# Kernel optimization log

Measured on AMD Instinct MI355X. Metric: run time of the kernel, lower is better.

The kernel has to match this reference:

```python
import jax, jax.numpy as jnp
import numpy as np

B, S, D, H, K, R = 16, 512, 768, 12, 16, 32
NS = 128  # LSH sample size = min(128, S//2)
HD = D // H

def _ln(t, g, b):
    m = t.mean(-1, keepdims=True)
    v = t.var(-1, keepdims=True)
    return (t - m) / jnp.sqrt(v + 1e-5) * g + b

def setup_inputs() -> dict:
    key = jax.random.key(0)
    ks = jax.random.split(key, 16)
    n = lambda k, shp: jax.random.normal(k, shp, jnp.float32) * 0.02
    return {
        'x': jax.random.normal(ks[0], (B, S, D), jnp.float32),
        'sample_idx': jax.random.randint(ks[1], (NS,), 0, S, jnp.int32),
        'w1': n(ks[2], (6, D // 4)), 'b1': jnp.zeros(D // 4, jnp.float32),
        'w2': n(ks[3], (D // 4, R)), 'b2': jnp.zeros(R, jnp.float32),
        'wd0': n(ks[4], (R, R)), 'bd0': jnp.zeros(R, jnp.float32),
        'wd1': n(ks[5], (R, R)), 'bd1': jnp.zeros(R, jnp.float32),
        'in_proj_w': n(ks[6], (D, 3 * D)), 'in_proj_b': jnp.zeros(3 * D, jnp.float32),
        'out_proj_w': n(ks[7], (D, D)), 'out_proj_b': jnp.zeros(D, jnp.float32),
        'topo_w': n(ks[8], (R, D)), 'topo_b': jnp.zeros(D, jnp.float32),
        'topo_gate': jnp.float32(0.1),
        'ln1_g': jnp.ones(D, jnp.float32), 'ln1_b': jnp.zeros(D, jnp.float32),
        'ln2_g': jnp.ones(D, jnp.float32), 'ln2_b': jnp.zeros(D, jnp.float32),
        'ffn_w1': n(ks[9], (D, 2 * D)), 'ffn_b1': jnp.zeros(2 * D, jnp.float32),
        'ffn_w2': n(ks[10], (2 * D, D)), 'ffn_b2': jnp.zeros(D, jnp.float32),
    }

def reference(x, sample_idx, w1, b1, w2, b2, wd0, bd0, wd1, bd1,
              in_proj_w, in_proj_b, out_proj_w, out_proj_b,
              topo_w, topo_b, topo_gate, ln1_g, ln1_b, ln2_g, ln2_b,
              ffn_w1, ffn_b1, ffn_w2, ffn_b2):
    # --- FastLSH._lsh_knn (S > 256 path): cdist to 128 sampled tokens + topk smallest ---
    s = jnp.take(x, sample_idx, axis=1)                                   # [B,NS,D]
    d2 = (jnp.sum(x * x, -1)[:, :, None] + jnp.sum(s * s, -1)[:, None, :]
          - 2.0 * jnp.einsum('bnd,bmd->bnm', x, s))                       # [B,S,NS]
    dist = jnp.sqrt(jnp.maximum(d2, 0.0))
    neg_top, _nbr = jax.lax.top_k(-dist, K)
    knn_dist = -neg_top                                                   # [B,S,K]
    # --- SimplifiedPersistenceComputer: scalar stats per batch (torch uses .item(), detached) ---
    df = knn_dist.reshape(B, -1)
    mean = df.mean(1); std = df.std(1, ddof=1)                            # torch.std is unbiased
    mn = df.min(1); mx = df.max(1)
    stats0 = jax.lax.stop_gradient(
        jnp.stack([mean, std, mn, mx, mean / 2, std / 2], -1))            # [B,6]
    # --- FastPersistenceLandscape: only dim-0 landscape feeds attention ---
    land0 = (jax.nn.relu(stats0 @ w1 + b1) @ w2 + b2) @ wd0 + bd0         # [B,R]
    # --- TopologicalAttention: MHA self-attention + gated topo embedding ---
    qkv = x @ in_proj_w + in_proj_b                                       # [B,S,3D]
    q, k, v = jnp.split(qkv, 3, axis=-1)
    hsplit = lambda t: t.reshape(B, S, H, HD).transpose(0, 2, 1, 3)
    q, k, v = hsplit(q), hsplit(k), hsplit(v)
    p = jax.nn.softmax(jnp.einsum('bhqd,bhkd->bhqk', q, k) / jnp.sqrt(jnp.float32(HD)), -1)
    o = jnp.einsum('bhqk,bhkd->bhqd', p, v).transpose(0, 2, 1, 3).reshape(B, S, D)
    attn = o @ out_proj_w + out_proj_b
    topo = land0 @ topo_w + topo_b                                        # [B,D]
    attn_out = attn + topo_gate * topo[:, None, :]
    # --- post-norm residual + FFN (GELU exact) ---
    x1 = _ln(x + attn_out, ln1_g, ln1_b)
    ffn = jax.nn.gelu(x1 @ ffn_w1 + ffn_b1, approximate=False) @ ffn_w2 + ffn_b2
    return _ln(x1 + ffn, ln2_g, ln2_b)
```

## Files before the change

### kernel.cpp

```cpp
#include <hip/hip_runtime.h>
#include <math.h>

#define Bz 16
#define Sz 512
#define Dz 768
#define Hz 12
#define HDz 64
#define Kz 16
#define NSz 128
#define Rz 32

typedef __attribute__((ext_vector_type(4))) float f32x4;
typedef __attribute__((ext_vector_type(8))) short bf16x8;

__device__ __forceinline__ unsigned short f2bf(float f) {
    unsigned u = __float_as_uint(f);
    return (unsigned short)((u + 0x7fffu + ((u >> 16) & 1u)) >> 16);
}
__device__ __forceinline__ float bf2f(unsigned short s) {
    return __uint_as_float(((unsigned)s) << 16);
}
__device__ __forceinline__ unsigned pk2(float a, float b) {
    return (unsigned)f2bf(a) | ((unsigned)f2bf(b) << 16);
}
__device__ __forceinline__ void gload_lds16(const void* g, void* l) {
    __builtin_amdgcn_global_load_lds(
        (const __attribute__((address_space(1))) unsigned int*)g,
        (__attribute__((address_space(3))) unsigned int*)l, 16, 0, 0);
}

__global__ __launch_bounds__(256) void xrn_k(const float* __restrict__ x, short* __restrict__ xb,
                                             float* __restrict__ xsq) {
    int wv = threadIdx.x >> 6, lane = threadIdx.x & 63;
    int row = blockIdx.x * 4 + wv;
    const float* r = x + (size_t)row * Dz;
    unsigned long long* dst = (unsigned long long*)(xb + (size_t)row * Dz);
    float s = 0.f;
#pragma unroll
    for (int j = 0; j < 3; j++) {
        float4 v = ((const float4*)r)[lane + j * 64];
        s += v.x * v.x + v.y * v.y + v.z * v.z + v.w * v.w;
        dst[lane + j * 64] = (unsigned long long)pk2(v.x, v.y) | ((unsigned long long)pk2(v.z, v.w) << 32);
    }
#pragma unroll
    for (int off = 32; off > 0; off >>= 1) s += __shfl_xor(s, off, 64);
    if (lane == 0) xsq[row] = s;
}

__global__ __launch_bounds__(256) void wtrans_k(const float* __restrict__ src, short* __restrict__ dst,
                                                int K, int N) {
    __shared__ float t[64][65];
    int k0 = blockIdx.y * 64, n0 = blockIdx.x * 64;
#pragma unroll
    for (int i = 0; i < 16; i++) {
        int e = threadIdx.x + 256 * i;
        int kk = e >> 6, nn = e & 63;
        t[kk][nn] = src[(size_t)(k0 + kk) * N + n0 + nn];
    }
    __syncthreads();
#pragma unroll
    for (int i = 0; i < 16; i++) {
        int e = threadIdx.x + 256 * i;
        int nn = e >> 6, kk = e & 63;
        dst[(size_t)(n0 + nn) * K + k0 + kk] = (short)f2bf(t[kk][nn]);
    }
}

__global__ __launch_bounds__(256) void dist_k(const float* __restrict__ x, const int* __restrict__ sidx,
                                              const float* __restrict__ xsq, float* __restrict__ D) {
    __shared__ float Xs[16][65];
    __shared__ float Ss[16][65];
    int b = blockIdx.z, st = blockIdx.y, jt = blockIdx.x;
    int tx = threadIdx.x & 15, ty = threadIdx.x >> 4;
    const float* xb = x + (size_t)b * Sz * Dz;
    float acc[4][4] = {};
    for (int k0 = 0; k0 < Dz; k0 += 16) {
#pragma unroll
        for (int i = 0; i < 4; i++) {
            int e = threadIdx.x + 256 * i;
            int m = e >> 4, kk = e & 15;
            Xs[kk][m] = xb[(size_t)(st * 64 + m) * Dz + k0 + kk];
            Ss[kk][m] = xb[(size_t)sidx[jt * 64 + m] * Dz + k0 + kk];
        }
        __syncthreads();
#pragma unroll
        for (int kk = 0; kk < 16; kk++) {
            float a[4], bb[4];
#pragma unroll
            for (int i = 0; i < 4; i++) a[i] = Xs[kk][ty * 4 + i];
#pragma unroll
            for (int j = 0; j < 4; j++) bb[j] = Ss[kk][tx * 4 + j];
#pragma unroll
            for (int i = 0; i < 4; i++)
#pragma unroll
                for (int j = 0; j < 4; j++) acc[i][j] += a[i] * bb[j];
        }
        __syncthreads();
    }
#pragma unroll
    for (int i = 0; i < 4; i++) {
        int s = st * 64 + ty * 4 + i;
#pragma unroll
        for (int j = 0; j < 4; j++) {
            int jj = jt * 64 + tx * 4 + j;
            float d2 = xsq[b * Sz + s] + xsq[b * Sz + sidx[jj]] - 2.f * acc[i][j];
            D[((size_t)b * Sz + s) * NSz + jj] = sqrtf(fmaxf(d2, 0.f));
        }
    }
}

__global__ __launch_bounds__(128) void knnstat_k(const float* __restrict__ D, float4* __restrict__ rowred) {
    __shared__ float dv[NSz];
    __shared__ float red[NSz], red2[NSz];
    __shared__ float rmin, rmax;
    int tid = threadIdx.x, row = blockIdx.x;
    float dist = D[(size_t)row * NSz + tid];
    dv[tid] = dist;
    __syncthreads();
    int rank = 0;
#pragma unroll 8
    for (int j = 0; j < NSz; j++) {
        float o = dv[j];
        rank += (o < dist) || (o == dist && j < tid);
    }
    if (rank == 0) rmin = dist;
    if (rank == Kz - 1) rmax = dist;
    red[tid] = (rank < Kz) ? dist : 0.f;
    red2[tid] = (rank < Kz) ? dist * dist : 0.f;
    __syncthreads();
    for (int st = 64; st > 0; st >>= 1) {
        if (tid < st) { red[tid] += red[tid + st]; red2[tid] += red2[tid + st]; }
        __syncthreads();
    }
    if (tid == 0) rowred[row] = make_float4(red[0], red2[0], rmin, rmax);
}

__global__ __launch_bounds__(256) void land_topo_k(const float4* __restrict__ rowred,
                                                   const float* __restrict__ w1, const float* __restrict__ b1,
                                                   const float* __restrict__ w2, const float* __restrict__ b2,
                                                   const float* __restrict__ wd0, const float* __restrict__ bd0,
                                                   const float* __restrict__ topo_w, const float* __restrict__ topo_b,
                                                   const float* gate, float* __restrict__ topo_add) {
    __shared__ float4 red4[256];
    __shared__ float st[6];
    __shared__ float h[Dz / 4];
    __shared__ float l2[Rz];
    __shared__ float land[Rz];
    int b = blockIdx.x, tid = threadIdx.x;
    float4 a = rowred[b * Sz + tid];
    float4 c = rowred[b * Sz + 256 + tid];
    float4 r;
    r.x = a.x + c.x; r.y = a.y + c.y;
    r.z = fminf(a.z, c.z); r.w = fmaxf(a.w, c.w);
    red4[tid] = r;
    __syncthreads();
    for (int stp = 128; stp > 0; stp >>= 1) {
        if (tid < stp) {
            float4 p = red4[tid], q = red4[tid + stp];
            p.x += q.x; p.y += q.y; p.z = fminf(p.z, q.z); p.w = fmaxf(p.w, q.w);
            red4[tid] = p;
        }
        __syncthreads();
    }
    if (tid == 0) {
        const double N = (double)(Sz * Kz);
        double sum = (double)red4[0].x, sumsq = (double)red4[0].y;
        double mean = sum / N;
        double var = (sumsq - N * mean * mean) / (N - 1.0);
        float sd = (float)sqrt(fmax(var, 0.0));
        float m = (float)mean;
        st[0] = m; st[1] = sd;
        st[2] = red4[0].z; st[3] = red4[0].w;
        st[4] = m * 0.5f; st[5] = sd * 0.5f;
    }
    __syncthreads();
    if (tid < Dz / 4) {
        float a1 = b1[tid];
#pragma unroll
        for (int i = 0; i < 6; i++) a1 += st[i] * w1[i * (Dz / 4) + tid];
        h[tid] = fmaxf(a1, 0.f);
    }
    __syncthreads();
    if (tid < Rz) {
        float a1 = b2[tid];
        for (int i = 0; i < Dz / 4; i++) a1 += h[i] * w2[i * Rz + tid];
        l2[tid] = a1;
    }
    __syncthreads();
    if (tid < Rz) {
        float a1 = bd0[tid];
#pragma unroll
        for (int i = 0; i < Rz; i++) a1 += l2[i] * wd0[i * Rz + tid];
        land[tid] = a1;
    }
    __syncthreads();
    float g = gate[0];
    for (int d = tid; d < Dz; d += 256) {
        float a1 = topo_b[d];
#pragma unroll
        for (int i = 0; i < Rz; i++) a1 += land[i] * topo_w[i * Dz + d];
        topo_add[b * Dz + d] = g * a1;
    }
}

__device__ __forceinline__ void stage_tile(const short* gbase, int ldk, int row0, int k0,
                                           short* ldsbase, int w, int l) {
#pragma unroll
    for (int c = 0; c < 2; c++) {
        int r = c * 64 + w * 16 + (l >> 2);
        int qg = (l & 3) ^ ((r >> 1) & 3);
        const short* src = gbase + (size_t)(row0 + r) * ldk + k0 + qg * 8;
        gload_lds16(src, ldsbase + (c * 4 + w) * 512);
    }
}

template <int EPI>
__global__ __launch_bounds__(256) void mgemm_k(const short* __restrict__ A, const short* __restrict__ BT,
                                               const float* __restrict__ bias,
                                               float* __restrict__ C, short* __restrict__ Cb,
                                               int N, int Kd,
                                               short* __restrict__ qo, short* __restrict__ ko,
                                               short* __restrict__ vT) {
    __shared__ short lds[2][2][4096];
    int tid = threadIdx.x, w = tid >> 6, l = tid & 63;
    int m0 = blockIdx.y * 128, n0 = blockIdx.x * 128;
    int wr = w >> 1, wc = w & 1, g = l >> 4, ql = l & 15;
    f32x4 acc[4][4];
#pragma unroll
    for (int i = 0; i < 4; i++)
#pragma unroll
        for (int j = 0; j < 4; j++) acc[i][j] = (f32x4){0.f, 0.f, 0.f, 0.f};
    stage_tile(A, Kd, m0, 0, lds[0][0], w, l);
    stage_tile(BT, Kd, n0, 0, lds[0][1], w, l);
    __syncthreads();
    int nst = Kd / 32;
    for (int t = 0; t < nst; t++) {
        int buf = t & 1;
        if (t + 1 < nst) {
            stage_tile(A, Kd, m0, (t + 1) * 32, lds[buf ^ 1][0], w, l);
            stage_tile(BT, Kd, n0, (t + 1) * 32, lds[buf ^ 1][1], w, l);
        }
        bf16x8 af[4], bfr[4];
#pragma unroll
        for (int i = 0; i < 4; i++) {
            int r = wr * 64 + i * 16 + ql;
            af[i] = *(const bf16x8*)((const char*)lds[buf][0] + r * 64 + ((g ^ ((r >> 1) & 3)) << 4));
        }
#pragma unroll
        for (int j = 0; j < 4; j++) {
            int r = wc * 64 + j * 16 + ql;
            bfr[j] = *(const bf16x8*)((const char*)lds[buf][1] + r * 64 + ((g ^ ((r >> 1) & 3)) << 4));
        }
#pragma unroll
        for (int i = 0; i < 4; i++)
#pragma unroll
            for (int j = 0; j < 4; j++)
                acc[i][j] = __builtin_amdgcn_mfma_f32_16x16x32_bf16(af[i], bfr[j], acc[i][j], 0, 0, 0);
        __syncthreads();
    }

    if (EPI == 0) {
#pragma unroll
        for (int i = 0; i < 4; i++) {
            int rowb = m0 + wr * 64 + i * 16 + g * 4;
#pragma unroll
            for (int j = 0; j < 4; j++) {
                int col = n0 + wc * 64 + j * 16 + ql;
                float bsv = bias[col];
#pragma unroll
                for (int r = 0; r < 4; r++)
                    C[(size_t)(rowb + r) * N + col] = acc[i][j][r] + bsv;
            }
        }
    } else {
        short* cl = (short*)lds;
        const int part = (EPI == 2) ? (n0 / Dz) : 0;
        const bool cm = (EPI == 2) && (part == 2);
        if (!cm) {
#pragma unroll
            for (int i = 0; i < 4; i++) {
#pragma unroll
                for (int j = 0; j < 4; j++) {
                    int colL = wc * 64 + j * 16 + ql;
                    float bsv = bias[n0 + colL];
#pragma unroll
                    for (int r = 0; r < 4; r++) {
                        int rowL = wr * 64 + i * 16 + g * 4 + r;
                        float val = acc[i][j][r] + bsv;
                        if (EPI == 1) val = 0.5f * val * (1.f + erff(val * 0.70710678118654752f));
                        cl[rowL * 128 + (((colL >> 3) ^ (rowL & 15)) << 3) + (colL & 7)] = (short)f2bf(val);
                    }
                }
            }
        } else {
#pragma unroll
            for (int i = 0; i < 4; i++) {
#pragma unroll
                for (int j = 0; j < 4; j++) {
                    int colL = wc * 64 + j * 16 + ql;
                    float bsv = bias[n0 + colL];
                    int row4 = wr * 64 + i * 16 + g * 4;
                    unsigned long long u =
                        (unsigned long long)pk2(acc[i][j][0] + bsv, acc[i][j][1] + bsv)
                      | ((unsigned long long)pk2(acc[i][j][2] + bsv, acc[i][j][3] + bsv) << 32);
                    *(unsigned long long*)((char*)cl +
                        colL * 256 + (((row4 >> 3) ^ (colL & 15)) << 4) + (row4 & 7) * 2) = u;
                }
            }
        }
        __syncthreads();
#pragma unroll
        for (int it = 0; it < 8; it++) {
            int c = tid + 256 * it;
            int a = c >> 4, sl = c & 15;
            bf16x8 vv = *(const bf16x8*)(cl + a * 128 + ((sl ^ (a & 15)) << 3));
            if (EPI == 1) {
                *(bf16x8*)(Cb + (size_t)(m0 + a) * N + n0 + sl * 8) = vv;
            } else if (!cm) {
                int rr = m0 + a;
                int b = rr >> 9, s = rr & 511;
                int h = ((n0 % Dz) >> 6) + (sl >> 3);
                short* dst = part ? ko : qo;
                *(bf16x8*)(dst + (((size_t)(b * Hz + h)) * Sz + s) * HDz + (sl & 7) * 8) = vv;
            } else {
                int wi = (n0 - 2 * Dz) + a;
                int h = wi >> 6, hd = wi & 63;
                int b = m0 >> 9, s0 = (m0 & 511) + sl * 8;
                *(bf16x8*)(vT + ((size_t)(b * Hz + h) * HDz + hd) * Sz + s0) = vv;
            }
        }
    }
}

__global__ __launch_bounds__(256, 4) void attn4_k(const short* __restrict__ Q, const short* __restrict__ Kt,
                                                  const short* __restrict__ Vt, short* __restrict__ O) {
    __shared__ short kl[2][4096];
    __shared__ short vl[2][4096];
    __shared__ char plds[4][2048];
    int tid = threadIdx.x, w = tid >> 6, l = tid & 63;
    int bh = blockIdx.x % (Bz * Hz), qt = blockIdx.x / (Bz * Hz);
    int g = l >> 4, ql = l & 15;
    const short* qb = Q + (size_t)bh * (Sz * HDz) + (size_t)(qt * 64 + w * 16) * HDz;
    const short* kb = Kt + (size_t)bh * (Sz * HDz);
    const short* vb = Vt + (size_t)bh * (HDz * Sz);
    bf16x8 qf0 = *(const bf16x8*)(qb + (size_t)ql * HDz + g * 8);
    bf16x8 qf1 = *(const bf16x8*)(qb + (size_t)ql * HDz + 32 + g * 8);
    f32x4 oa[4];
#pragma unroll
    for (int m = 0; m < 4; m++) oa[m] = (f32x4){0.f, 0.f, 0.f, 0.f};
    float psum = 0.f;

    auto stage = [&](int c, int bb) {
#pragma unroll
        for (int it = 0; it < 2; it++) {
            int i = (it * 4 + w) * 64 + l;
            int row = i >> 3;
            int ss = (i & 7) ^ (row & 7);
            gload_lds16(kb + (size_t)(c * 64 + row) * HDz + ss * 8,
                        (char*)kl[bb] + (it * 4 + w) * 1024);
            gload_lds16(vb + (size_t)row * Sz + c * 64 + ss * 8,
                        (char*)vl[bb] + (it * 4 + w) * 1024);
        }
    };

    stage(0, 0);
    __syncthreads();
    char* pw = plds[w];
#pragma unroll
    for (int c = 0; c < 8; c++) {
        int cur = c & 1;
        if (c < 7) stage(c + 1, cur ^ 1);
        const char* kc = (const char*)kl[cur];
        const char* vc = (const char*)vl[cur];
#pragma unroll
        for (int tl = 0; tl < 4; tl++) {
            int row = tl * 16 + ql;
            bf16x8 a0 = *(const bf16x8*)(kc + row * 128 + ((g ^ (ql & 7)) << 4));
            bf16x8 a1 = *(const bf16x8*)(kc + row * 128 + (((4 + g) ^ (ql & 7)) << 4));
            f32x4 s4 = (f32x4){0.f, 0.f, 0.f, 0.f};
            s4 = __builtin_amdgcn_mfma_f32_16x16x32_bf16(a0, qf0, s4, 0, 0, 0);
            s4 = __builtin_amdgcn_mfma_f32_16x16x32_bf16(a1, qf1, s4, 0, 0, 0);
            float e0 = __expf(s4[0] * 0.125f);
            float e1 = __expf(s4[1] * 0.125f);
            float e2 = __expf(s4[2] * 0.125f);
            float e3 = __expf(s4[3] * 0.125f);
            psum += (e0 + e1) + (e2 + e3);
            int slot = (tl * 2 + (g >> 1)) ^ (ql & 7);
            *(unsigned long long*)(pw + ql * 128 + slot * 16 + (g & 1) * 8)
                = (unsigned long long)pk2(e0, e1) | ((unsigned long long)pk2(e2, e3) << 32);
        }
#pragma unroll
        for (int s = 0; s < 2; s++) {
            int slot = (s * 4 + g) ^ (ql & 7);
            bf16x8 pb = *(const bf16x8*)(pw + ql * 128 + slot * 16);
#pragma unroll
            for (int m = 0; m < 4; m++) {
                int row = m * 16 + ql;
                bf16x8 va = *(const bf16x8*)(vc + row * 128 + (((s * 4 + g) ^ (ql & 7)) << 4));
                oa[m] = __builtin_amdgcn_mfma_f32_16x16x32_bf16(va, pb, oa[m], 0, 0, 0);
            }
        }
        __syncthreads();
    }
    psum += __shfl_xor(psum, 16, 64);
    psum += __shfl_xor(psum, 32, 64);
    float inv = 1.f / psum;
    int b = bh / Hz, h = bh % Hz;
    int s = qt * 64 + w * 16 + ql;
#pragma unroll
    for (int m = 0; m < 4; m++)
#pragma unroll
        for (int j = 0; j < 2; j++) {
            float v0 = oa[m][j * 2] * inv, v1 = oa[m][j * 2 + 1] * inv;
            unsigned u = pk2(v0, v1);
            int d = h * 64 + m * 16 + g * 4 + j * 2;
            *(unsigned*)((char*)O + 2 * ((size_t)(b * Sz + s) * Dz + d)) = u;
        }
}

__global__ __launch_bounds__(256) void ln1_k(const float* __restrict__ x, const float* __restrict__ ap,
                                             const float* __restrict__ topo,
                                             const float* __restrict__ gam, const float* __restrict__ bet,
                                             short* __restrict__ x1b) {
    __shared__ float buf[Dz];
    __shared__ float red[256];
    int row = blockIdx.x, tid = threadIdx.x, b = row >> 9;
    float s = 0.f;
    for (int i = tid; i < Dz; i += 256) {
        float vv = x[(size_t)row * Dz + i] + ap[(size_t)row * Dz + i] + topo[b * Dz + i];
        buf[i] = vv; s += vv;
    }
    red[tid] = s; __syncthreads();
    for (int st = 128; st > 0; st >>= 1) { if (tid < st) red[tid] += red[tid + st]; __syncthreads(); }
    float mean = red[0] / (float)Dz;
    __syncthreads();
    float s2 = 0.f;
    for (int i = tid; i < Dz; i += 256) { float d = buf[i] - mean; s2 += d * d; }
    red[tid] = s2; __syncthreads();
    for (int st = 128; st > 0; st >>= 1) { if (tid < st) red[tid] += red[tid + st]; __syncthreads(); }
    float inv = 1.f / sqrtf(red[0] / (float)Dz + 1e-5f);
    for (int i = tid; i < Dz; i += 256)
        x1b[(size_t)row * Dz + i] = (short)f2bf((buf[i] - mean) * inv * gam[i] + bet[i]);
}

__global__ __launch_bounds__(256) void ln2_k(const short* __restrict__ x1b, const float* __restrict__ f2,
                                             const float* __restrict__ gam, const float* __restrict__ bet,
                                             float* __restrict__ out) {
    __shared__ float buf[Dz];
    __shared__ float red[256];
    int row = blockIdx.x, tid = threadIdx.x;
    float s = 0.f;
    for (int i = tid; i < Dz; i += 256) {
        float vv = bf2f((unsigned short)x1b[(size_t)row * Dz + i]) + f2[(size_t)row * Dz + i];
        buf[i] = vv; s += vv;
    }
    red[tid] = s; __syncthreads();
    for (int st = 128; st > 0; st >>= 1) { if (tid < st) red[tid] += red[tid + st]; __syncthreads(); }
    float mean = red[0] / (float)Dz;
    __syncthreads();
    float s2 = 0.f;
    for (int i = tid; i < Dz; i += 256) { float d = buf[i] - mean; s2 += d * d; }
    red[tid] = s2; __syncthreads();
    for (int st = 128; st > 0; st >>= 1) { if (tid < st) red[tid] += red[tid + st]; __syncthreads(); }
    float inv = 1.f / sqrtf(red[0] / (float)Dz + 1e-5f);
    for (int i = tid; i < Dz; i += 256)
        out[(size_t)row * Dz + i] = (buf[i] - mean) * inv * gam[i] + bet[i];
}

extern "C" void kernel_launch(void* const* d_in, const int* in_sizes, int n_in,
                              void* d_out, int out_size, void* d_ws, size_t ws_size,
                              hipStream_t stream) {
    const float* x          = (const float*)d_in[0];
    const int*   sidx       = (const int*)d_in[1];
    const float* w1         = (const float*)d_in[2];
    const float* b1         = (const float*)d_in[3];
    const float* w2         = (const float*)d_in[4];
    const float* b2         = (const float*)d_in[5];
    const float* wd0        = (const float*)d_in[6];
    const float* bd0        = (const float*)d_in[7];
    const float* in_proj_w  = (const float*)d_in[10];
    const float* in_proj_b  = (const float*)d_in[11];
    const float* out_proj_w = (const float*)d_in[12];
    const float* out_proj_b = (const float*)d_in[13];
    const float* topo_w     = (const float*)d_in[14];
    const float* topo_b     = (const float*)d_in[15];
    const float* gate       = (const float*)d_in[16];
    const float* ln1_g      = (const float*)d_in[17];
    const float* ln1_b      = (const float*)d_in[18];
    const float* ln2_g      = (const float*)d_in[19];
    const float* ln2_b      = (const float*)d_in[20];
    const float* ffn_w1     = (const float*)d_in[21];
    const float* ffn_b1     = (const float*)d_in[22];
    const float* ffn_w2     = (const float*)d_in[23];
    const float* ffn_b2     = (const float*)d_in[24];

    char* w = (char*)d_ws;
    float4* rowred = (float4*)(w + 0);
    float*  xsq    = (float*)(w + 131072);
    float*  topo_add = (float*)(w + 163840);
    size_t off = 212992;
    short* wT_ip = (short*)(w + off); off += (size_t)3 * Dz * Dz * 2;
    short* wT_op = (short*)(w + off); off += (size_t)Dz * Dz * 2;
    short* wT_f1 = (short*)(w + off); off += (size_t)2 * Dz * Dz * 2;
    short* wT_f2 = (short*)(w + off); off += (size_t)2 * Dz * Dz * 2;
    float* Dd    = (float*)(w + off); off += (size_t)Bz * Sz * NSz * 4;
    char*  qkv0  = w + off;           off += (size_t)3 * Bz * Sz * Dz * 2;
    short* qbuf  = (short*)qkv0;
    short* kbuf  = (short*)(qkv0 + (size_t)Bz * Sz * Dz * 2);
    short* vTbuf = (short*)(qkv0 + (size_t)2 * Bz * Sz * Dz * 2);
    short* x1b   = (short*)qkv0;
    short* hb    = (short*)(qkv0 + (size_t)Bz * Sz * Dz * 2);
    short* xb    = (short*)(w + off); off += (size_t)Bz * Sz * Dz * 2;
    short* ob    = xb;
    float* bigF  = (float*)(w + off); off += (size_t)Bz * Sz * Dz * 4;

    const int M = Bz * Sz;

    xrn_k<<<M / 4, 256, 0, stream>>>(x, xb, xsq);
    wtrans_k<<<dim3(3 * Dz / 64, Dz / 64), 256, 0, stream>>>(in_proj_w, wT_ip, Dz, 3 * Dz);
    wtrans_k<<<dim3(Dz / 64, Dz / 64), 256, 0, stream>>>(out_proj_w, wT_op, Dz, Dz);
    wtrans_k<<<dim3(2 * Dz / 64, Dz / 64), 256, 0, stream>>>(ffn_w1, wT_f1, Dz, 2 * Dz);
    wtrans_k<<<dim3(Dz / 64, 2 * Dz / 64), 256, 0, stream>>>(ffn_w2, wT_f2, 2 * Dz, Dz);
    dist_k<<<dim3(NSz / 64, Sz / 64, Bz), 256, 0, stream>>>(x, sidx, xsq, Dd);
    knnstat_k<<<M, 128, 0, stream>>>(Dd, rowred);
    land_topo_k<<<Bz, 256, 0, stream>>>(rowred, w1, b1, w2, b2,
                                        wd0, bd0, topo_w, topo_b, gate, topo_add);
    mgemm_k<2><<<dim3(3 * Dz / 128, M / 128), 256, 0, stream>>>(xb, wT_ip, in_proj_b,
                                                                nullptr, nullptr, 3 * Dz, Dz,
                                                                qbuf, kbuf, vTbuf);
    attn4_k<<<Bz * Hz * 8, 256, 0, stream>>>(qbuf, kbuf, vTbuf, ob);
    mgemm_k<0><<<dim3(Dz / 128, M / 128), 256, 0, stream>>>(ob, wT_op, out_proj_b,
                                                            bigF, nullptr, Dz, Dz,
                                                            nullptr, nullptr, nullptr);
    ln1_k<<<M, 256, 0, stream>>>(x, bigF, topo_add, ln1_g, ln1_b, x1b);
    mgemm_k<1><<<dim3(2 * Dz / 128, M / 128), 256, 0, stream>>>(x1b, wT_f1, ffn_b1,
                                                                nullptr, hb, 2 * Dz, Dz,
                                                                nullptr, nullptr, nullptr);
    mgemm_k<0><<<dim3(Dz / 128, M / 128), 256, 0, stream>>>(hb, wT_f2, ffn_b2,
                                                            bigF, nullptr, Dz, 2 * Dz,
                                                            nullptr, nullptr, nullptr);
    ln2_k<<<M, 256, 0, stream>>>(x1b, bigF, ln2_g, ln2_b, (float*)d_out);
}
```

Before: 444.4 us.

## Merge prep kernels, use MFMA GEMM for distances, XCD-swizzle tiles, bf16 GEMM outputs

Merges the four weight-transpose launches and a gather of the sampled tokens into bf16 into a single prep kernel. The fp32 CUDA-core cdist kernel is replaced by the bf16 MFMA GEMM, with a new epilogue that computes sqrt distances. GEMM launches become 1D grids with a block-index remap that spreads consecutive tiles across the eight XCDs, and the out-proj and FFN2 outputs are stored as bf16 instead of fp32 to halve that traffic. The bf16 distance products may reorder near-tied neighbours in top-k, and the bf16 residual inputs slightly reduce accuracy.

```diff
diff --git a/kernel.cpp b/kernel.cpp
--- a/kernel.cpp
+++ b/kernel.cpp
@@ -47,64 +47,56 @@
     if (lane == 0) xsq[row] = s;
 }
 
-__global__ __launch_bounds__(256) void wtrans_k(const float* __restrict__ src, short* __restrict__ dst,
-                                                int K, int N) {
-    __shared__ float t[64][65];
-    int k0 = blockIdx.y * 64, n0 = blockIdx.x * 64;
+__device__ __forceinline__ void wtrans_body(const float* __restrict__ src, short* __restrict__ dst,
+                                            int K, int N, int k0, int n0, int tid,
+                                            float (*t)[65]) {
 #pragma unroll
     for (int i = 0; i < 16; i++) {
-        int e = threadIdx.x + 256 * i;
+        int e = tid + 256 * i;
         int kk = e >> 6, nn = e & 63;
         t[kk][nn] = src[(size_t)(k0 + kk) * N + n0 + nn];
     }
     __syncthreads();
 #pragma unroll
     for (int i = 0; i < 16; i++) {
-        int e = threadIdx.x + 256 * i;
+        int e = tid + 256 * i;
         int nn = e >> 6, kk = e & 63;
         dst[(size_t)(n0 + nn) * K + k0 + kk] = (short)f2bf(t[kk][nn]);
     }
 }
 
-__global__ __launch_bounds__(256) void dist_k(const float* __restrict__ x, const int* __restrict__ sidx,
-                                              const float* __restrict__ xsq, float* __restrict__ D) {
-    __shared__ float Xs[16][65];
-    __shared__ float Ss[16][65];
-    int b = blockIdx.z, st = blockIdx.y, jt = blockIdx.x;
-    int tx = threadIdx.x & 15, ty = threadIdx.x >> 4;
-    const float* xb = x + (size_t)b * Sz * Dz;
-    float acc[4][4] = {};
-    for (int k0 = 0; k0 < Dz; k0 += 16) {
-#pragma unroll
-        for (int i = 0; i < 4; i++) {
-            int e = threadIdx.x + 256 * i;
-            int m = e >> 4, kk = e & 15;
-            Xs[kk][m] = xb[(size_t)(st * 64 + m) * Dz + k0 + kk];
-            Ss[kk][m] = xb[(size_t)sidx[jt * 64 + m] * Dz + k0 + kk];
-        }
-        __syncthreads();
-#pragma unroll
-        for (int kk = 0; kk < 16; kk++) {
-            float a[4], bb[4];
-#pragma unroll
-            for (int i = 0; i < 4; i++) a[i] = Xs[kk][ty * 4 + i];
-#pragma unroll
-            for (int j = 0; j < 4; j++) bb[j] = Ss[kk][tx * 4 + j];
-#pragma unroll
-            for (int i = 0; i < 4; i++)
-#pragma unroll
-                for (int j = 0; j < 4; j++) acc[i][j] += a[i] * bb[j];
-        }
-        __syncthreads();
-    }
-#pragma unroll
-    for (int i = 0; i < 4; i++) {
-        int s = st * 64 + ty * 4 + i;
-#pragma unroll
-        for (int j = 0; j < 4; j++) {
-            int jj = jt * 64 + tx * 4 + j;
-            float d2 = xsq[b * Sz + s] + xsq[b * Sz + sidx[jj]] - 2.f * acc[i][j];
-            D[((size_t)b * Sz + s) * NSz + jj] = sqrtf(fmaxf(d2, 0.f));
+__global__ __launch_bounds__(256) void prep_k(const float* __restrict__ ipw, const float* __restrict__ opw,
+                                              const float* __restrict__ f1w, const float* __restrict__ f2w,
+                                              short* __restrict__ wT_ip, short* __restrict__ wT_op,
+                                              short* __restrict__ wT_f1, short* __restrict__ wT_f2,
+                                              const float* __restrict__ x, const int* __restrict__ sidx,
+                                              short* __restrict__ scb) {
+    __shared__ float t[64][65];
+    int bid = blockIdx.x, tid = threadIdx.x;
+    if (bid < 432) {
+        int lo = bid, tx = lo % 36, ty = lo / 36;
+        wtrans_body(ipw, wT_ip, Dz, 3 * Dz, ty * 64, tx * 64, tid, t);
+    } else if (bid < 576) {
+        int lo = bid - 432, tx = lo % 12, ty = lo / 12;
+        wtrans_body(opw, wT_op, Dz, Dz, ty * 64, tx * 64, tid, t);
+    } else if (bid < 864) {
+        int lo = bid - 576, tx = lo % 24, ty = lo / 24;
+        wtrans_body(f1w, wT_f1, Dz, 2 * Dz, ty * 64, tx * 64, tid, t);
+    } else if (bid < 1152) {
+        int lo = bid - 864, tx = lo % 12, ty = lo / 12;
+        wtrans_body(f2w, wT_f2, 2 * Dz, Dz, ty * 64, tx * 64, tid, t);
+    } else {
+        int gb = bid - 1152;
+        int row = gb * 16 + (tid >> 4);
+        int b = row >> 7, jj = row & 127;
+        const float* src = x + ((size_t)(b * Sz) + sidx[jj]) * Dz;
+        unsigned long long* dr = (unsigned long long*)(scb + (size_t)row * Dz);
+        int l16 = tid & 15;
+#pragma unroll
+        for (int j = 0; j < 12; j++) {
+            int idx = j * 16 + l16;
+            float4 v = ((const float4*)src)[idx];
+            dr[idx] = (unsigned long long)pk2(v.x, v.y) | ((unsigned long long)pk2(v.z, v.w) << 32);
         }
     }
 }
@@ -218,12 +210,17 @@
 __global__ __launch_bounds__(256) void mgemm_k(const short* __restrict__ A, const short* __restrict__ BT,
                                                const float* __restrict__ bias,
                                                float* __restrict__ C, short* __restrict__ Cb,
-                                               int N, int Kd,
+                                               int N, int Kd, int gx,
                                                short* __restrict__ qo, short* __restrict__ ko,
-                                               short* __restrict__ vT) {
+                                               short* __restrict__ vT,
+                                               const int* __restrict__ sidx, const float* __restrict__ xsq) {
     __shared__ short lds[2][2][4096];
     int tid = threadIdx.x, w = tid >> 6, l = tid & 63;
-    int m0 = blockIdx.y * 128, n0 = blockIdx.x * 128;
+    int nwg = gridDim.x, q = nwg >> 3;
+    int orig = (blockIdx.x & 7) * q + (blockIdx.x >> 3);
+    int m0 = (orig / gx) * 128, n0 = (orig % gx) * 128;
+    const short* BTb = BT;
+    if (EPI == 4) BTb += (size_t)(m0 >> 9) * NSz * Kd;
     int wr = w >> 1, wc = w & 1, g = l >> 4, ql = l & 15;
     f32x4 acc[4][4];
 #pragma unroll
@@ -231,14 +228,14 @@
 #pragma unroll
         for (int j = 0; j < 4; j++) acc[i][j] = (f32x4){0.f, 0.f, 0.f, 0.f};
     stage_tile(A, Kd, m0, 0, lds[0][0], w, l);
-    stage_tile(BT, Kd, n0, 0, lds[0][1], w, l);
+    stage_tile(BTb, Kd, n0, 0, lds[0][1], w, l);
     __syncthreads();
     int nst = Kd / 32;
     for (int t = 0; t < nst; t++) {
         int buf = t & 1;
         if (t + 1 < nst) {
             stage_tile(A, Kd, m0, (t + 1) * 32, lds[buf ^ 1][0], w, l);
-            stage_tile(BT, Kd, n0, (t + 1) * 32, lds[buf ^ 1][1], w, l);
+            stage_tile(BTb, Kd, n0, (t + 1) * 32, lds[buf ^ 1][1], w, l);
         }
         bf16x8 af[4], bfr[4];
 #pragma unroll
@@ -259,17 +256,20 @@
         __syncthreads();
     }
 
-    if (EPI == 0) {
+    if (EPI == 4) {
 #pragma unroll
         for (int i = 0; i < 4; i++) {
             int rowb = m0 + wr * 64 + i * 16 + g * 4;
 #pragma unroll
             for (int j = 0; j < 4; j++) {
-                int col = n0 + wc * 64 + j * 16 + ql;
-                float bsv = bias[col];
-#pragma unroll
-                for (int r = 0; r < 4; r++)
-                    C[(size_t)(rowb + r) * N + col] = acc[i][j][r] + bsv;
+                int col = wc * 64 + j * 16 + ql;
+                float ssq = xsq[((rowb >> 9) << 9) + sidx[col]];
+#pragma unroll
+                for (int r = 0; r < 4; r++) {
+                    int row = rowb + r;
+                    float d2 = xsq[row] + ssq - 2.f * acc[i][j][r];
+                    C[(size_t)row * NSz + col] = sqrtf(fmaxf(d2, 0.f));
+                }
             }
         }
     } else {
@@ -314,7 +314,7 @@
             int c = tid + 256 * it;
             int a = c >> 4, sl = c & 15;
             bf16x8 vv = *(const bf16x8*)(cl + a * 128 + ((sl ^ (a & 15)) << 3));
-            if (EPI == 1) {
+            if (EPI == 1 || EPI == 3) {
                 *(bf16x8*)(Cb + (size_t)(m0 + a) * N + n0 + sl * 8) = vv;
             } else if (!cm) {
                 int rr = m0 + a;
@@ -418,7 +418,7 @@
         }
 }
 
-__global__ __launch_bounds__(256) void ln1_k(const float* __restrict__ x, const float* __restrict__ ap,
+__global__ __launch_bounds__(256) void ln1_k(const float* __restrict__ x, const short* __restrict__ ap,
                                              const float* __restrict__ topo,
                                              const float* __restrict__ gam, const float* __restrict__ bet,
                                              short* __restrict__ x1b) {
@@ -427,7 +427,7 @@
     int row = blockIdx.x, tid = threadIdx.x, b = row >> 9;
     float s = 0.f;
     for (int i = tid; i < Dz; i += 256) {
-        float vv = x[(size_t)row * Dz + i] + ap[(size_t)row * Dz + i] + topo[b * Dz + i];
+        float vv = x[(size_t)row * Dz + i] + bf2f((unsigned short)ap[(size_t)row * Dz + i]) + topo[b * Dz + i];
         buf[i] = vv; s += vv;
     }
     red[tid] = s; __syncthreads();
@@ -443,7 +443,7 @@
         x1b[(size_t)row * Dz + i] = (short)f2bf((buf[i] - mean) * inv * gam[i] + bet[i]);
 }
 
-__global__ __launch_bounds__(256) void ln2_k(const short* __restrict__ x1b, const float* __restrict__ f2,
+__global__ __launch_bounds__(256) void ln2_k(const short* __restrict__ x1b, const short* __restrict__ f2,
                                              const float* __restrict__ gam, const float* __restrict__ bet,
                                              float* __restrict__ out) {
     __shared__ float buf[Dz];
@@ -451,7 +451,7 @@
     int row = blockIdx.x, tid = threadIdx.x;
     float s = 0.f;
     for (int i = tid; i < Dz; i += 256) {
-        float vv = bf2f((unsigned short)x1b[(size_t)row * Dz + i]) + f2[(size_t)row * Dz + i];
+        float vv = bf2f((unsigned short)x1b[(size_t)row * Dz + i]) + bf2f((unsigned short)f2[(size_t)row * Dz + i]);
         buf[i] = vv; s += vv;
     }
     red[tid] = s; __syncthreads();
@@ -503,6 +503,7 @@
     short* wT_op = (short*)(w + off); off += (size_t)Dz * Dz * 2;
     short* wT_f1 = (short*)(w + off); off += (size_t)2 * Dz * Dz * 2;
     short* wT_f2 = (short*)(w + off); off += (size_t)2 * Dz * Dz * 2;
+    short* scb   = (short*)(w + off); off += (size_t)Bz * NSz * Dz * 2;
     float* Dd    = (float*)(w + off); off += (size_t)Bz * Sz * NSz * 4;
     char*  qkv0  = w + off;           off += (size_t)3 * Bz * Sz * Dz * 2;
     short* qbuf  = (short*)qkv0;
@@ -512,32 +513,32 @@
     short* hb    = (short*)(qkv0 + (size_t)Bz * Sz * Dz * 2);
     short* xb    = (short*)(w + off); off += (size_t)Bz * Sz * Dz * 2;
     short* ob    = xb;
-    float* bigF  = (float*)(w + off); off += (size_t)Bz * Sz * Dz * 4;
+    short* apb   = (short*)(w + off); off += (size_t)Bz * Sz * Dz * 2;
+    short* f2b   = (short*)(w + off); off += (size_t)Bz * Sz * Dz * 2;
 
     const int M = Bz * Sz;
 
     xrn_k<<<M / 4, 256, 0, stream>>>(x, xb, xsq);
-    wtrans_k<<<dim3(3 * Dz / 64, Dz / 64), 256, 0, stream>>>(in_proj_w, wT_ip, Dz, 3 * Dz);
-    wtrans_k<<<dim3(Dz / 64, Dz / 64), 256, 0, stream>>>(out_proj_w, wT_op, Dz, Dz);
-    wtrans_k<<<dim3(2 * Dz / 64, Dz / 64), 256, 0, stream>>>(ffn_w1, wT_f1, Dz, 2 * Dz);
-    wtrans_k<<<dim3(Dz / 64, 2 * Dz / 64), 256, 0, stream>>>(ffn_w2, wT_f2, 2 * Dz, Dz);
-    dist_k<<<dim3(NSz / 64, Sz / 64, Bz), 256, 0, stream>>>(x, sidx, xsq, Dd);
+    prep_k<<<1280, 256, 0, stream>>>(in_proj_w, out_proj_w, ffn_w1, ffn_w2,
+                                     wT_ip, wT_op, wT_f1, wT_f2, x, sidx, scb);
+    mgemm_k<4><<<M / 128, 256, 0, stream>>>(xb, scb, nullptr, Dd, nullptr,
+                                            NSz, Dz, 1, nullptr, nullptr, nullptr, sidx, xsq);
     knnstat_k<<<M, 128, 0, stream>>>(Dd, rowred);
     land_topo_k<<<Bz, 256, 0, stream>>>(rowred, w1, b1, w2, b2,
                                         wd0, bd0, topo_w, topo_b, gate, topo_add);
-    mgemm_k<2><<<dim3(3 * Dz / 128, M / 128), 256, 0, stream>>>(xb, wT_ip, in_proj_b,
-                                                                nullptr, nullptr, 3 * Dz, Dz,
-                                                                qbuf, kbuf, vTbuf);
+    mgemm_k<2><<<(3 * Dz / 128) * (M / 128), 256, 0, stream>>>(xb, wT_ip, in_proj_b,
+                                                               nullptr, nullptr, 3 * Dz, Dz, 3 * Dz / 128,
+                                                               qbuf, kbuf, vTbuf, nullptr, nullptr);
     attn4_k<<<Bz * Hz * 8, 256, 0, stream>>>(qbuf, kbuf, vTbuf, ob);
-    mgemm_k<0><<<dim3(Dz / 128, M / 128), 256, 0, stream>>>(ob, wT_op, out_proj_b,
-                                                            bigF, nullptr, Dz, Dz,
-                                                            nullptr, nullptr, nullptr);
-    ln1_k<<<M, 256, 0, stream>>>(x, bigF, topo_add, ln1_g, ln1_b, x1b);
-    mgemm_k<1><<<dim3(2 * Dz / 128, M / 128), 256, 0, stream>>>(x1b, wT_f1, ffn_b1,
-                                                                nullptr, hb, 2 * Dz, Dz,
-                                                                nullptr, nullptr, nullptr);
-    mgemm_k<0><<<dim3(Dz / 128, M / 128), 256, 0, stream>>>(hb, wT_f2, ffn_b2,
-                                                            bigF, nullptr, Dz, 2 * Dz,
-                                                            nullptr, nullptr, nullptr);
-    ln2_k<<<M, 256, 0, stream>>>(x1b, bigF, ln2_g, ln2_b, (float*)d_out);
-}
+    mgemm_k<3><<<(Dz / 128) * (M / 128), 256, 0, stream>>>(ob, wT_op, out_proj_b,
+                                                           nullptr, apb, Dz, Dz, Dz / 128,
+                                                           nullptr, nullptr, nullptr, nullptr, nullptr);
+    ln1_k<<<M, 256, 0, stream>>>(x, apb, topo_add, ln1_g, ln1_b, x1b);
+    mgemm_k<1><<<(2 * Dz / 128) * (M / 128), 256, 0, stream>>>(x1b, wT_f1, ffn_b1,
+                                                               nullptr, hb, 2 * Dz, Dz, 2 * Dz / 128,
+                                                               nullptr, nullptr, nullptr, nullptr, nullptr);
+    mgemm_k<3><<<(Dz / 128) * (M / 128), 256, 0, stream>>>(hb, wT_f2, ffn_b2,
+                                                           nullptr, f2b, Dz, 2 * Dz, Dz / 128,
+                                                           nullptr, nullptr, nullptr, nullptr, nullptr);
+    ln2_k<<<M, 256, 0, stream>>>(x1b, f2b, ln2_g, ln2_b, (float*)d_out);
+}
```

Result: faster. 399.1 us (-10.2%).
